# Kernel optimization log

Measured on AMD Instinct MI355X. Metric: run time of the kernel, lower is better.

## Reference

```python
import jax, jax.numpy as jnp
import numpy as np

B, S, D = 4, 4096, 256
UNITS = 256
NRF = 256  # n_random_features (must equal units for the score matmul)


def setup_inputs() -> dict:
    key = jax.random.key(0)
    ks = jax.random.split(key, 10)
    s = 1.0 / np.sqrt(D)
    return {
        "query": jax.random.normal(ks[0], (B, S, D), jnp.float32),
        "value": jax.random.normal(ks[1], (B, S, D), jnp.float32),
        "Wq": jax.random.normal(ks[2], (D, UNITS), jnp.float32) * s,
        "bq": jnp.zeros((UNITS,), jnp.float32),
        "Wk": jax.random.normal(ks[3], (D, UNITS), jnp.float32) * s,
        "bk": jnp.zeros((UNITS,), jnp.float32),
        "Wv": jax.random.normal(ks[4], (D, UNITS), jnp.float32) * s,
        "bv": jnp.zeros((UNITS,), jnp.float32),
        # random-feature map params (non-trainable in original, init 'random_normal' ~ stddev 0.05)
        "Wr": jax.random.normal(ks[5], (UNITS, NRF), jnp.float32) * 0.05,
        "br": jax.random.normal(ks[6], (NRF,), jnp.float32) * 0.05,
    }


def reference(query, value, Wq, bq, Wk, bk, Wv, bv, Wr, br):
    # Dense projections
    Q = jnp.einsum("bsd,du->bsu", query, Wq) + bq   # [B,S,U]
    K = jnp.einsum("bsd,du->bsu", value, Wk) + bk   # [B,S,U]
    V = jnp.einsum("bsd,du->bsu", value, Wv) + bv   # [B,S,U]
    # random-feature kernel map on K
    K_hat = jnp.cos(jnp.einsum("bsu,ur->bsr", K, Wr) + br)  # [B,S,R]
    # attention: Q @ K_hat^T -> softmax -> @ V
    scores = jnp.einsum("bqr,bkr->bqk", Q, K_hat)    # [B,S,S]
    probs = jax.nn.softmax(scores, axis=-1)
    return jnp.einsum("bqk,bku->bqu", probs, V)      # [B,S,U]
```

## Files before the change

### kernel.cpp

```cpp
#include <hip/hip_runtime.h>
#include <hip/hip_bf16.h>

typedef _Float16 f16;
typedef _Float16 f16x8 __attribute__((ext_vector_type(8)));
typedef _Float16 f16x4 __attribute__((ext_vector_type(4)));
typedef float f32x4 __attribute__((ext_vector_type(4)));
typedef float f32x16 __attribute__((ext_vector_type(16)));

#define MFMA1632(a, b, c) __builtin_amdgcn_mfma_f32_16x16x32_f16(a, b, c, 0, 0, 0)
#define MFMA3216(a, b, c) __builtin_amdgcn_mfma_f32_32x32x16_f16(a, b, c, 0, 0, 0)

#define GLL16(g, l)                                                        \
    __builtin_amdgcn_global_load_lds(                                      \
        (const __attribute__((address_space(1))) void*)(g),                \
        (__attribute__((address_space(3))) void*)(l), 16, 0, 0)

static constexpr int S  = 4096;
static constexpr int NB = 4;

__global__ void wconv4_kernel(const float* __restrict__ W0, const float* __restrict__ W1,
                              const float* __restrict__ W2, const float* __restrict__ W3,
                              f16* __restrict__ T0, f16* __restrict__ T1,
                              f16* __restrict__ T2, f16* __restrict__ T3) {
    int j = blockIdx.x >> 8;
    int k = blockIdx.x & 255;
    int n = threadIdx.x;
    const float* W = (j == 0) ? W0 : (j == 1) ? W1 : (j == 2) ? W2 : W3;
    f16*         T = (j == 0) ? T0 : (j == 1) ? T1 : (j == 2) ? T2 : T3;
    T[n * 256 + k] = (f16)W[k * 256 + n];
}

__global__ __launch_bounds__(256) void qproj_kernel(
    const float* __restrict__ Af, const f16* __restrict__ Wt,
    const float* __restrict__ bias, f16* __restrict__ O)
{
    int mbase = blockIdx.x * 32;
    int tid = threadIdx.x;
    int w = tid >> 6, l = tid & 63;
    int lr = l & 15, lg = l >> 4;
    int nbase = w * 64;

    f32x4 acc[2][4];
#pragma unroll
    for (int mf = 0; mf < 2; ++mf)
#pragma unroll
        for (int nf = 0; nf < 4; ++nf) acc[mf][nf] = f32x4{0.f, 0.f, 0.f, 0.f};

#pragma unroll
    for (int ks = 0; ks < 8; ++ks) {
        int kof = ks * 32 + lg * 8;
        f16x8 a[2], b[4];
#pragma unroll
        for (int mf = 0; mf < 2; ++mf) {
            int row = mbase + mf * 16 + lr;
            const float4* p = (const float4*)(Af + row * 256 + kof);
            float4 x0 = p[0], x1 = p[1];
            f16x8 t;
            t[0] = (f16)x0.x; t[1] = (f16)x0.y; t[2] = (f16)x0.z; t[3] = (f16)x0.w;
            t[4] = (f16)x1.x; t[5] = (f16)x1.y; t[6] = (f16)x1.z; t[7] = (f16)x1.w;
            a[mf] = t;
        }
#pragma unroll
        for (int nf = 0; nf < 4; ++nf) {
            int col = nbase + nf * 16 + lr;
            b[nf] = *(const f16x8*)(Wt + col * 256 + kof);
        }
#pragma unroll
        for (int mf = 0; mf < 2; ++mf)
#pragma unroll
            for (int nf = 0; nf < 4; ++nf)
                acc[mf][nf] = MFMA1632(a[mf], b[nf], acc[mf][nf]);
    }

#pragma unroll
    for (int mf = 0; mf < 2; ++mf) {
#pragma unroll
        for (int nf = 0; nf < 4; ++nf) {
            int col = nbase + nf * 16 + lr;
            float bv = bias[col];
#pragma unroll
            for (int r = 0; r < 4; ++r) {
                int row = mbase + mf * 16 + lg * 4 + r;
                O[row * 256 + col] = (f16)(acc[mf][nf][r] + bv);
            }
        }
    }
}

__global__ __launch_bounds__(512) void kvhproj_kernel(
    const float* __restrict__ Af,
    const f16* __restrict__ WkT, const f16* __restrict__ WvT,
    const f16* __restrict__ WrT,
    const float* __restrict__ bk, const float* __restrict__ bv,
    const float* __restrict__ br,
    f16* __restrict__ Hf, f16* __restrict__ VtF)
{
    __shared__ f16 KS[32][264];

    int mbase = blockIdx.x * 32;
    int tid = threadIdx.x;
    int w = tid >> 6, l = tid & 63;
    int lr = l & 15, lg = l >> 4;
    int path = w >> 2;
    int nbase = (w & 3) * 64;
    const f16* Wt = path ? WvT : WkT;
    const float* bias = path ? bv : bk;

    f32x4 acc[2][4];
#pragma unroll
    for (int mf = 0; mf < 2; ++mf)
#pragma unroll
        for (int nf = 0; nf < 4; ++nf) acc[mf][nf] = f32x4{0.f, 0.f, 0.f, 0.f};

#pragma unroll
    for (int ks = 0; ks < 8; ++ks) {
        int kof = ks * 32 + lg * 8;
        f16x8 a[2], b[4];
#pragma unroll
        for (int mf = 0; mf < 2; ++mf) {
            int row = mbase + mf * 16 + lr;
            const float4* p = (const float4*)(Af + row * 256 + kof);
            float4 x0 = p[0], x1 = p[1];
            f16x8 t;
            t[0] = (f16)x0.x; t[1] = (f16)x0.y; t[2] = (f16)x0.z; t[3] = (f16)x0.w;
            t[4] = (f16)x1.x; t[5] = (f16)x1.y; t[6] = (f16)x1.z; t[7] = (f16)x1.w;
            a[mf] = t;
        }
#pragma unroll
        for (int nf = 0; nf < 4; ++nf) {
            int col = nbase + nf * 16 + lr;
            b[nf] = *(const f16x8*)(Wt + col * 256 + kof);
        }
#pragma unroll
        for (int mf = 0; mf < 2; ++mf)
#pragma unroll
            for (int nf = 0; nf < 4; ++nf)
                acc[mf][nf] = MFMA1632(a[mf], b[nf], acc[mf][nf]);
    }

#pragma unroll
    for (int mf = 0; mf < 2; ++mf) {
#pragma unroll
        for (int nf = 0; nf < 4; ++nf) {
            int col = nbase + nf * 16 + lr;
            float bv2 = bias[col];
            if (path == 0) {
#pragma unroll
                for (int r = 0; r < 4; ++r)
                    KS[mf * 16 + lg * 4 + r][col] = (f16)(acc[mf][nf][r] + bv2);
            } else {
                int bi = mbase >> 12;
                int s  = (mbase & (S - 1)) + mf * 16 + lg * 4;
                f16x4 v;
#pragma unroll
                for (int r = 0; r < 4; ++r) v[r] = (f16)(acc[mf][nf][r] + bv2);
                *(f16x4*)(VtF + ((bi * 256 + col) * S + s)) = v;
            }
        }
    }
    __syncthreads();

    f32x4 acc2[2][2];
#pragma unroll
    for (int mf = 0; mf < 2; ++mf)
#pragma unroll
        for (int nf = 0; nf < 2; ++nf) acc2[mf][nf] = f32x4{0.f, 0.f, 0.f, 0.f};

#pragma unroll
    for (int ks = 0; ks < 8; ++ks) {
        int kof = ks * 32 + lg * 8;
        f16x8 a[2], b[2];
#pragma unroll
        for (int mf = 0; mf < 2; ++mf)
            a[mf] = *(const f16x8*)&KS[mf * 16 + lr][kof];
#pragma unroll
        for (int nf = 0; nf < 2; ++nf) {
            int col = w * 32 + nf * 16 + lr;
            b[nf] = *(const f16x8*)(WrT + col * 256 + kof);
        }
#pragma unroll
        for (int mf = 0; mf < 2; ++mf)
#pragma unroll
            for (int nf = 0; nf < 2; ++nf)
                acc2[mf][nf] = MFMA1632(a[mf], b[nf], acc2[mf][nf]);
    }

#pragma unroll
    for (int mf = 0; mf < 2; ++mf) {
#pragma unroll
        for (int nf = 0; nf < 2; ++nf) {
            int col = w * 32 + nf * 16 + lr;
            float bv2 = br[col];
#pragma unroll
            for (int r = 0; r < 4; ++r) {
                int row = mbase + mf * 16 + lg * 4 + r;
                Hf[row * 256 + col] = (f16)cosf(acc2[mf][nf][r] + bv2);
            }
        }
    }
}

__global__ __launch_bounds__(512, 2) void attn_kernel(
    const f16* __restrict__ Qf, const f16* __restrict__ Hf,
    const f16* __restrict__ Vt, float* __restrict__ Out)
{
    __shared__ f16 KhS[128 * 256];
    __shared__ f16 VtS[256 * 128];
    __shared__ f16 PSh[64 * 128];
    __shared__ float auxF[2][4][32];
    __shared__ float auxT[2][32];
    __shared__ float auxC[2][32];
    __shared__ int flagLds;

    int bid = blockIdx.x;
    int b   = (bid >> 1) & 3;
    int qi  = ((bid >> 3) << 1) | (bid & 1);
    int qbase = qi * 64;

    int tid = threadIdx.x;
    int w  = tid >> 6, l = tid & 63;
    int qh = w >> 2;
    int kg = w & 3;
    int lm = l & 31;
    int h  = l >> 5;

    const f16* Hbase = Hf + (size_t)b * S * 256;
    const f16* Vbase = Vt + (size_t)b * 256 * S;

    f16x8 qf[16];
    {
        const f16* qp = Qf + (size_t)(b * S + qbase + qh * 32 + lm) * 256 + h * 8;
#pragma unroll
        for (int s = 0; s < 16; ++s) qf[s] = *(const f16x8*)(qp + s * 16);
    }

    f32x16 oac0, oac1;
#pragma unroll
    for (int i = 0; i < 16; ++i) { oac0[i] = 0.f; oac1[i] = 0.f; }
    float mrun = -1e30f, lsum = 0.f;

    if (tid == 0) flagLds = 0;

#pragma unroll
    for (int i = 0; i < 8; ++i) {
        int c = i * 512 + tid;
        int row = c >> 5, ch = c & 31;
        GLL16(Hbase + (size_t)row * 256 + ((ch ^ (row & 31)) * 8),
              KhS + (size_t)(i * 4096 + w * 512));
    }
#pragma unroll
    for (int i = 0; i < 8; ++i) {
        int d  = w * 32 + i * 4 + (l >> 4);
        int cp = l & 15;
        GLL16(Vbase + (size_t)d * S + ((cp ^ (d & 15)) * 8),
              VtS + (size_t)(w * 4096 + i * 512));
    }
    __syncthreads();

    const int NT = S / 128;
    for (int t = 0; t < NT; ++t) {
        int kt = t * 128;

        f32x16 s0, s1;
#pragma unroll
        for (int i = 0; i < 16; ++i) { s0[i] = 0.f; s1[i] = 0.f; }
        {
            const f16* kb = KhS + (size_t)(kg * 32 + lm) * 256;
            __builtin_amdgcn_s_setprio(1);
#pragma unroll
            for (int s = 0; s < 16; s += 2) {
                f16x8 ka0 = *(const f16x8*)(kb + ((2 * s + h) ^ lm) * 8);
                f16x8 ka1 = *(const f16x8*)(kb + ((2 * s + 2 + h) ^ lm) * 8);
                s0 = MFMA3216(ka0, qf[s], s0);
                s1 = MFMA3216(ka1, qf[s + 1], s1);
            }
            __builtin_amdgcn_s_setprio(0);
        }
        f32x16 sc;
#pragma unroll
        for (int i = 0; i < 16; ++i) sc[i] = s0[i] + s1[i];

        int need = 0;
#pragma unroll
        for (int i = 0; i < 16; ++i) need |= (sc[i] > mrun + 8.f) ? 1 : 0;
        if (__any(need)) { if (l == 0) flagLds = 1; }
        __syncthreads();

        if (t + 1 < NT) {
#pragma unroll
            for (int i = 0; i < 8; ++i) {
                int c = i * 512 + tid;
                int row = c >> 5, ch = c & 31;
                GLL16(Hbase + (size_t)(kt + 128 + row) * 256 + ((ch ^ (row & 31)) * 8),
                      KhS + (size_t)(i * 4096 + w * 512));
            }
        }

        if (flagLds) {
            float mx = sc[0];
#pragma unroll
            for (int i = 1; i < 16; ++i) mx = fmaxf(mx, sc[i]);
            mx = fmaxf(mx, __shfl_xor(mx, 32));
            if (l < 32) auxF[qh][kg][lm] = mx;
            __syncthreads();
            float mnew = fmaxf(fmaxf(auxF[qh][0][lm], auxF[qh][1][lm]),
                               fmaxf(auxF[qh][2][lm], auxF[qh][3][lm]));
            mnew = fmaxf(mrun, mnew);
            float corr = __expf(mrun - mnew);
            lsum *= corr;
            if (kg == 0 && l < 32) auxT[qh][lm] = corr;
            mrun = mnew;
            if (tid == 0) flagLds = 0;
            __syncthreads();
#pragma unroll
            for (int i = 0; i < 16; ++i) {
                int cr = (i & 3) + 8 * (i >> 2) + 4 * h;
                oac0[i] *= auxT[0][cr];
                oac1[i] *= auxT[1][cr];
            }
        }

        {
            f16* pw = PSh + (size_t)(qh * 32 + lm) * 128;
            int key = lm & 15;
#pragma unroll
            for (int b4 = 0; b4 < 4; ++b4) {
                float p0 = __expf(sc[b4 * 4 + 0] - mrun);
                float p1 = __expf(sc[b4 * 4 + 1] - mrun);
                float p2 = __expf(sc[b4 * 4 + 2] - mrun);
                float p3 = __expf(sc[b4 * 4 + 3] - mrun);
                lsum += (p0 + p1) + (p2 + p3);
                f16x4 pv;
                pv[0] = (f16)p0; pv[1] = (f16)p1; pv[2] = (f16)p2; pv[3] = (f16)p3;
                *(f16x4*)(pw + ((4 * kg + b4) ^ key) * 8 + 4 * h) = pv;
            }
        }

        asm volatile("s_waitcnt lgkmcnt(0)" ::: "memory");
        __builtin_amdgcn_s_barrier();

        {
            const f16* pb0 = PSh + (size_t)lm * 128;
            const f16* pb1 = PSh + (size_t)(32 + lm) * 128;
            const f16* vb  = VtS + (size_t)(w * 32 + lm) * 128;
            int kp = lm & 15;
            __builtin_amdgcn_s_setprio(1);
#pragma unroll
            for (int s = 0; s < 8; ++s) {
                int lc = 2 * s + h;
                f16x8 pa0 = *(const f16x8*)(pb0 + (lc ^ kp) * 8);
                f16x8 pa1 = *(const f16x8*)(pb1 + (lc ^ kp) * 8);
                f16x8 vv  = *(const f16x8*)(vb  + (lc ^ kp) * 8);
                oac0 = MFMA3216(pa0, vv, oac0);
                oac1 = MFMA3216(pa1, vv, oac1);
            }
            __builtin_amdgcn_s_setprio(0);
        }

        if (t + 1 < NT) {
#pragma unroll
            for (int i = 0; i < 8; ++i) {
                int d  = w * 32 + i * 4 + (l >> 4);
                int cp = l & 15;
                GLL16(Vbase + (size_t)d * S + (kt + 128) + ((cp ^ (d & 15)) * 8),
                      VtS + (size_t)(w * 4096 + i * 512));
            }
        }

        asm volatile("s_waitcnt vmcnt(8)" ::: "memory");
        __builtin_amdgcn_s_barrier();
    }

    lsum += __shfl_xor(lsum, 32);
    if (l < 32) auxF[qh][kg][lm] = lsum;
    __syncthreads();
    if (kg == 0 && l < 32) {
        float dsum = auxF[qh][0][lm] + auxF[qh][1][lm] +
                     auxF[qh][2][lm] + auxF[qh][3][lm];
        auxC[qh][lm] = 1.0f / dsum;
    }
    __syncthreads();

    float* Ob = Out + (size_t)(b * S + qbase) * 256 + w * 32 + lm;
#pragma unroll
    for (int i = 0; i < 16; ++i) {
        int cr = (i & 3) + 8 * (i >> 2) + 4 * h;
        Ob[(size_t)cr * 256]        = oac0[i] * auxC[0][cr];
        Ob[(size_t)(32 + cr) * 256] = oac1[i] * auxC[1][cr];
    }
}

extern "C" void kernel_launch(void* const* d_in, const int* in_sizes, int n_in,
                              void* d_out, int out_size, void* d_ws, size_t ws_size,
                              hipStream_t stream)
{
    const float* query = (const float*)d_in[0];
    const float* value = (const float*)d_in[1];
    const float* Wq    = (const float*)d_in[2];
    const float* bq    = (const float*)d_in[3];
    const float* Wk    = (const float*)d_in[4];
    const float* bk    = (const float*)d_in[5];
    const float* Wv    = (const float*)d_in[6];
    const float* bv    = (const float*)d_in[7];
    const float* Wr    = (const float*)d_in[8];
    const float* br    = (const float*)d_in[9];
    float* out = (float*)d_out;

    char* ws = (char*)d_ws;
    size_t off = 0;
    auto alloc = [&](size_t bytes) -> char* {
        char* p = ws + off;
        off += (bytes + 255) & ~(size_t)255;
        return p;
    };
    f16* WqT = (f16*)alloc((size_t)65536 * 2);
    f16* WkT = (f16*)alloc((size_t)65536 * 2);
    f16* WvT = (f16*)alloc((size_t)65536 * 2);
    f16* WrT = (f16*)alloc((size_t)65536 * 2);
    f16* Qf  = (f16*)alloc((size_t)NB * S * 256 * 2);
    f16* Hf  = (f16*)alloc((size_t)NB * S * 256 * 2);
    f16* VtF = (f16*)alloc((size_t)NB * S * 256 * 2);
    (void)ws_size; (void)in_sizes; (void)n_in; (void)out_size;

    wconv4_kernel<<<1024, 256, 0, stream>>>(Wq, Wk, Wv, Wr, WqT, WkT, WvT, WrT);

    qproj_kernel<<<512, 256, 0, stream>>>(query, WqT, bq, Qf);
    kvhproj_kernel<<<512, 512, 0, stream>>>(value, WkT, WvT, WrT, bk, bv, br, Hf, VtF);

    attn_kernel<<<256, 512, 0, stream>>>(Qf, Hf, VtF, out);
}
```

Baseline: 165.0 us.

## Keep P in registers, split keys per wave with local softmax and final reduction

The attention kernel now keeps the probability tile in registers, packing it with cvt_pkrtz and v_permlane32_swap so it can feed the PV MFMA directly instead of going through shared memory. Each wave owns a key slice and all 256 output columns (8 accumulators), tracks its own running max and sum, and reads V straight from global memory. The Kh tile is double-buffered. A final cross-wave reduction through LDS rescales and sums the partial outputs. This removes the PSh and VtS staging and most per-tile barriers, in exchange for much higher register pressure (128 accumulator floats per lane), uncached global V reads, and a costlier epilogue.

```diff
diff --git a/kernel.cpp b/kernel.cpp
--- a/kernel.cpp
+++ b/kernel.cpp
@@ -2,10 +2,12 @@
 #include <hip/hip_bf16.h>
 
 typedef _Float16 f16;
+typedef __fp16 fp16x2 __attribute__((ext_vector_type(2)));
 typedef _Float16 f16x8 __attribute__((ext_vector_type(8)));
 typedef _Float16 f16x4 __attribute__((ext_vector_type(4)));
 typedef float f32x4 __attribute__((ext_vector_type(4)));
 typedef float f32x16 __attribute__((ext_vector_type(16)));
+typedef int i32x4 __attribute__((ext_vector_type(4)));
 
 #define MFMA1632(a, b, c) __builtin_amdgcn_mfma_f32_16x16x32_f16(a, b, c, 0, 0, 0)
 #define MFMA3216(a, b, c) __builtin_amdgcn_mfma_f32_32x32x16_f16(a, b, c, 0, 0, 0)
@@ -17,6 +19,14 @@
 
 static constexpr int S  = 4096;
 static constexpr int NB = 4;
+
+static __device__ __forceinline__ int packi(float a, float b) {
+    fp16x2 t = __builtin_amdgcn_cvt_pkrtz(a, b);
+    return __builtin_bit_cast(int, t);
+}
+static __device__ __forceinline__ void plswap(int& a, int& b) {
+    asm volatile("v_permlane32_swap_b32 %0, %1" : "+v"(a), "+v"(b));
+}
 
 __global__ void wconv4_kernel(const float* __restrict__ W0, const float* __restrict__ W1,
                               const float* __restrict__ W2, const float* __restrict__ W3,
@@ -204,13 +214,9 @@
     const f16* __restrict__ Qf, const f16* __restrict__ Hf,
     const f16* __restrict__ Vt, float* __restrict__ Out)
 {
-    __shared__ f16 KhS[128 * 256];
-    __shared__ f16 VtS[256 * 128];
-    __shared__ f16 PSh[64 * 128];
-    __shared__ float auxF[2][4][32];
-    __shared__ float auxT[2][32];
-    __shared__ float auxC[2][32];
-    __shared__ int flagLds;
+    __shared__ __align__(16) f16 KhS[2][128 * 256];
+    __shared__ float auxM[2][4][32];
+    __shared__ float auxL[2][4][32];
 
     int bid = blockIdx.x;
     int b   = (bid >> 1) & 3;
@@ -234,38 +240,42 @@
         for (int s = 0; s < 16; ++s) qf[s] = *(const f16x8*)(qp + s * 16);
     }
 
-    f32x16 oac0, oac1;
-#pragma unroll
-    for (int i = 0; i < 16; ++i) { oac0[i] = 0.f; oac1[i] = 0.f; }
+    f32x16 oac[8];
+#pragma unroll
+    for (int d2 = 0; d2 < 8; ++d2)
+#pragma unroll
+        for (int i = 0; i < 16; ++i) oac[d2][i] = 0.f;
     float mrun = -1e30f, lsum = 0.f;
-
-    if (tid == 0) flagLds = 0;
 
 #pragma unroll
     for (int i = 0; i < 8; ++i) {
         int c = i * 512 + tid;
         int row = c >> 5, ch = c & 31;
         GLL16(Hbase + (size_t)row * 256 + ((ch ^ (row & 31)) * 8),
-              KhS + (size_t)(i * 4096 + w * 512));
-    }
-#pragma unroll
-    for (int i = 0; i < 8; ++i) {
-        int d  = w * 32 + i * 4 + (l >> 4);
-        int cp = l & 15;
-        GLL16(Vbase + (size_t)d * S + ((cp ^ (d & 15)) * 8),
-              VtS + (size_t)(w * 4096 + i * 512));
+              &KhS[0][(size_t)(i * 4096 + w * 512)]);
     }
     __syncthreads();
 
     const int NT = S / 128;
     for (int t = 0; t < NT; ++t) {
+        int cur = t & 1;
         int kt = t * 128;
+
+        if (t + 1 < NT) {
+#pragma unroll
+            for (int i = 0; i < 8; ++i) {
+                int c = i * 512 + tid;
+                int row = c >> 5, ch = c & 31;
+                GLL16(Hbase + (size_t)(kt + 128 + row) * 256 + ((ch ^ (row & 31)) * 8),
+                      &KhS[cur ^ 1][(size_t)(i * 4096 + w * 512)]);
+            }
+        }
 
         f32x16 s0, s1;
 #pragma unroll
         for (int i = 0; i < 16; ++i) { s0[i] = 0.f; s1[i] = 0.f; }
         {
-            const f16* kb = KhS + (size_t)(kg * 32 + lm) * 256;
+            const f16* kb = &KhS[cur][(size_t)(kg * 32 + lm) * 256];
             __builtin_amdgcn_s_setprio(1);
 #pragma unroll
             for (int s = 0; s < 16; s += 2) {
@@ -280,113 +290,94 @@
 #pragma unroll
         for (int i = 0; i < 16; ++i) sc[i] = s0[i] + s1[i];
 
-        int need = 0;
-#pragma unroll
-        for (int i = 0; i < 16; ++i) need |= (sc[i] > mrun + 8.f) ? 1 : 0;
-        if (__any(need)) { if (l == 0) flagLds = 1; }
+        float pm = sc[0];
+#pragma unroll
+        for (int i = 1; i < 16; ++i) pm = fmaxf(pm, sc[i]);
+        pm = fmaxf(pm, __shfl_xor(pm, 32));
+        if (pm > mrun + 8.f) {
+            float corr = __expf(mrun - pm);
+            lsum *= corr;
+#pragma unroll
+            for (int d2 = 0; d2 < 8; ++d2)
+#pragma unroll
+                for (int i = 0; i < 16; ++i) oac[d2][i] *= corr;
+            mrun = pm;
+        }
+        float p[16];
+#pragma unroll
+        for (int i = 0; i < 16; ++i) {
+            p[i] = __expf(sc[i] - mrun);
+            lsum += p[i];
+        }
+
+        f16x8 bf0, bf1;
+        {
+            int a0 = packi(p[0], p[1]),  a1 = packi(p[2], p[3]);
+            int b0 = packi(p[4], p[5]),  b1 = packi(p[6], p[7]);
+            plswap(a0, b0); plswap(a1, b1);
+            i32x4 v0; v0.x = a0; v0.y = a1; v0.z = b0; v0.w = b1;
+            bf0 = __builtin_bit_cast(f16x8, v0);
+            int c0 = packi(p[8], p[9]),   c1 = packi(p[10], p[11]);
+            int d0 = packi(p[12], p[13]), d1 = packi(p[14], p[15]);
+            plswap(c0, d0); plswap(c1, d1);
+            i32x4 v1; v1.x = c0; v1.y = c1; v1.z = d0; v1.w = d1;
+            bf1 = __builtin_bit_cast(f16x8, v1);
+        }
+
+        __builtin_amdgcn_s_setprio(1);
+#pragma unroll
+        for (int d2 = 0; d2 < 8; ++d2) {
+            const f16* vp = Vbase + (size_t)(d2 * 32 + lm) * S + kt + kg * 32 + h * 8;
+            f16x8 va0 = *(const f16x8*)(vp);
+            f16x8 va1 = *(const f16x8*)(vp + 16);
+            oac[d2] = MFMA3216(va0, bf0, oac[d2]);
+            oac[d2] = MFMA3216(va1, bf1, oac[d2]);
+        }
+        __builtin_amdgcn_s_setprio(0);
+
         __syncthreads();
-
-        if (t + 1 < NT) {
-#pragma unroll
-            for (int i = 0; i < 8; ++i) {
-                int c = i * 512 + tid;
-                int row = c >> 5, ch = c & 31;
-                GLL16(Hbase + (size_t)(kt + 128 + row) * 256 + ((ch ^ (row & 31)) * 8),
-                      KhS + (size_t)(i * 4096 + w * 512));
-            }
-        }
-
-        if (flagLds) {
-            float mx = sc[0];
-#pragma unroll
-            for (int i = 1; i < 16; ++i) mx = fmaxf(mx, sc[i]);
-            mx = fmaxf(mx, __shfl_xor(mx, 32));
-            if (l < 32) auxF[qh][kg][lm] = mx;
-            __syncthreads();
-            float mnew = fmaxf(fmaxf(auxF[qh][0][lm], auxF[qh][1][lm]),
-                               fmaxf(auxF[qh][2][lm], auxF[qh][3][lm]));
-            mnew = fmaxf(mrun, mnew);
-            float corr = __expf(mrun - mnew);
-            lsum *= corr;
-            if (kg == 0 && l < 32) auxT[qh][lm] = corr;
-            mrun = mnew;
-            if (tid == 0) flagLds = 0;
-            __syncthreads();
-#pragma unroll
-            for (int i = 0; i < 16; ++i) {
-                int cr = (i & 3) + 8 * (i >> 2) + 4 * h;
-                oac0[i] *= auxT[0][cr];
-                oac1[i] *= auxT[1][cr];
-            }
-        }
-
-        {
-            f16* pw = PSh + (size_t)(qh * 32 + lm) * 128;
-            int key = lm & 15;
-#pragma unroll
-            for (int b4 = 0; b4 < 4; ++b4) {
-                float p0 = __expf(sc[b4 * 4 + 0] - mrun);
-                float p1 = __expf(sc[b4 * 4 + 1] - mrun);
-                float p2 = __expf(sc[b4 * 4 + 2] - mrun);
-                float p3 = __expf(sc[b4 * 4 + 3] - mrun);
-                lsum += (p0 + p1) + (p2 + p3);
-                f16x4 pv;
-                pv[0] = (f16)p0; pv[1] = (f16)p1; pv[2] = (f16)p2; pv[3] = (f16)p3;
-                *(f16x4*)(pw + ((4 * kg + b4) ^ key) * 8 + 4 * h) = pv;
-            }
-        }
-
-        asm volatile("s_waitcnt lgkmcnt(0)" ::: "memory");
-        __builtin_amdgcn_s_barrier();
-
-        {
-            const f16* pb0 = PSh + (size_t)lm * 128;
-            const f16* pb1 = PSh + (size_t)(32 + lm) * 128;
-            const f16* vb  = VtS + (size_t)(w * 32 + lm) * 128;
-            int kp = lm & 15;
-            __builtin_amdgcn_s_setprio(1);
-#pragma unroll
-            for (int s = 0; s < 8; ++s) {
-                int lc = 2 * s + h;
-                f16x8 pa0 = *(const f16x8*)(pb0 + (lc ^ kp) * 8);
-                f16x8 pa1 = *(const f16x8*)(pb1 + (lc ^ kp) * 8);
-                f16x8 vv  = *(const f16x8*)(vb  + (lc ^ kp) * 8);
-                oac0 = MFMA3216(pa0, vv, oac0);
-                oac1 = MFMA3216(pa1, vv, oac1);
-            }
-            __builtin_amdgcn_s_setprio(0);
-        }
-
-        if (t + 1 < NT) {
-#pragma unroll
-            for (int i = 0; i < 8; ++i) {
-                int d  = w * 32 + i * 4 + (l >> 4);
-                int cp = l & 15;
-                GLL16(Vbase + (size_t)d * S + (kt + 128) + ((cp ^ (d & 15)) * 8),
-                      VtS + (size_t)(w * 4096 + i * 512));
-            }
-        }
-
-        asm volatile("s_waitcnt vmcnt(8)" ::: "memory");
-        __builtin_amdgcn_s_barrier();
     }
 
     lsum += __shfl_xor(lsum, 32);
-    if (l < 32) auxF[qh][kg][lm] = lsum;
+    if (h == 0) {
+        auxM[qh][kg][lm] = mrun;
+        auxL[qh][kg][lm] = lsum;
+    }
     __syncthreads();
-    if (kg == 0 && l < 32) {
-        float dsum = auxF[qh][0][lm] + auxF[qh][1][lm] +
-                     auxF[qh][2][lm] + auxF[qh][3][lm];
-        auxC[qh][lm] = 1.0f / dsum;
-    }
-    __syncthreads();
-
-    float* Ob = Out + (size_t)(b * S + qbase) * 256 + w * 32 + lm;
-#pragma unroll
-    for (int i = 0; i < 16; ++i) {
-        int cr = (i & 3) + 8 * (i >> 2) + 4 * h;
-        Ob[(size_t)cr * 256]        = oac0[i] * auxC[0][cr];
-        Ob[(size_t)(32 + cr) * 256] = oac1[i] * auxC[1][cr];
+
+    float mfin = fmaxf(fmaxf(auxM[qh][0][lm], auxM[qh][1][lm]),
+                       fmaxf(auxM[qh][2][lm], auxM[qh][3][lm]));
+    float den = auxL[qh][0][lm] * __expf(auxM[qh][0][lm] - mfin)
+              + auxL[qh][1][lm] * __expf(auxM[qh][1][lm] - mfin)
+              + auxL[qh][2][lm] * __expf(auxM[qh][2][lm] - mfin)
+              + auxL[qh][3][lm] * __expf(auxM[qh][3][lm] - mfin);
+    float myscale = __expf(mrun - mfin) / den;
+
+    float* LDSf = (float*)&KhS[0][0];
+    for (int pass = 0; pass < 2; ++pass) {
+        if (qh == pass) {
+#pragma unroll
+            for (int d2 = 0; d2 < 8; ++d2) {
+#pragma unroll
+                for (int i = 0; i < 16; ++i) {
+                    int crow = (i & 3) + 8 * (i >> 2) + 4 * h;
+                    LDSf[(kg * 32 + lm) * 256 + d2 * 32 + (crow ^ lm)] =
+                        oac[d2][i] * myscale;
+                }
+            }
+        }
+        __syncthreads();
+#pragma unroll
+        for (int it = 0; it < 16; ++it) {
+            int q   = it * 2 + h;
+            int col = w * 32 + (lm ^ q);
+            float v = LDSf[(0 * 32 + q) * 256 + col]
+                    + LDSf[(1 * 32 + q) * 256 + col]
+                    + LDSf[(2 * 32 + q) * 256 + col]
+                    + LDSf[(3 * 32 + q) * 256 + col];
+            Out[(size_t)(b * S + qbase + pass * 32 + q) * 256 + w * 32 + lm] = v;
+        }
+        __syncthreads();
     }
 }
 
```

Measured after the change: 287.6 us. +74.3%, slower.
